# Kernel optimization log

Measured on AMD Instinct MI355X. Metric: run time of the kernel, lower is better.

The kernel has to match this reference:

```python
import jax, jax.numpy as jnp
import numpy as np

EPS = 1e-5

def _bn_relu(x, gamma, beta):
    # BatchNorm2d in training mode: biased batch stats over (B, H, W)
    mu = jnp.mean(x, axis=(0, 2, 3), keepdims=True)
    var = jnp.mean((x - mu) ** 2, axis=(0, 2, 3), keepdims=True)
    xh = (x - mu) * jax.lax.rsqrt(var + EPS)
    return jax.nn.relu(xh * gamma[None, :, None, None] + beta[None, :, None, None])

def setup_inputs() -> dict:
    key = jax.random.key(0)
    ks = jax.random.split(key, 16)
    B, N, D = 4, 256, 256            # in_channels = 2*D = 512
    feats = jax.random.normal(ks[0], (B, 1 + 2 * N, D), dtype=jnp.float32)
    def lin(k, o, c):
        return jax.random.normal(k, (o, c), dtype=jnp.float32) * (1.0 / np.sqrt(c))
    return {
        "feats": feats,
        "W1": lin(ks[1], 256, 512), "b1": jnp.zeros((256,), jnp.float32),
        "g1": jnp.ones((256,), jnp.float32), "be1": jnp.zeros((256,), jnp.float32),
        "W2": lin(ks[2], 128, 256), "b2": jnp.zeros((128,), jnp.float32),
        "g2": jnp.ones((128,), jnp.float32), "be2": jnp.zeros((128,), jnp.float32),
        "W3": lin(ks[3], 64, 128), "b3": jnp.zeros((64,), jnp.float32),
        "g3": jnp.ones((64,), jnp.float32), "be3": jnp.zeros((64,), jnp.float32),
        "W4": lin(ks[4], 1, 64), "b4": jnp.zeros((1,), jnp.float32),
    }

def reference(feats, W1, b1, g1, be1, W2, b2, g2, be2, W3, b3, g3, be3, W4, b4):
    B, T, Dfull = feats.shape
    f = feats[:, 1:]                                  # [B, 2N, D]
    N = f.shape[1] // 2
    D = f.shape[2]
    f = f.reshape(B, N, 2, D).mean(axis=2)            # [B, N, D]
    fc = jnp.transpose(f, (0, 2, 1))                  # [B, D, N]
    # conv1(cat(x, t)) fused: first D input channels see f_i, last D see f_j
    a = jnp.einsum('oc,bcn->bon', W1[:, :D], fc)      # [B, 256, N]
    bpart = jnp.einsum('oc,bcn->bon', W1[:, D:], fc)  # [B, 256, N]
    h = a[:, :, :, None] + bpart[:, :, None, :] + b1[None, :, None, None]  # [B,256,N,N]
    h = _bn_relu(h, g1, be1)
    h = jnp.einsum('oc,bcij->boij', W2, h) + b2[None, :, None, None]
    h = _bn_relu(h, g2, be2)
    h = jnp.einsum('oc,bcij->boij', W3, h) + b3[None, :, None, None]
    h = _bn_relu(h, g3, be3)
    h = jnp.einsum('oc,bcij->boij', W4, h) + b4[None, :, None, None]
    return h[:, 0]                                    # [B, N, N]
```

## Files before the change

### kernel.cpp

```cpp
#include <hip/hip_runtime.h>
#include <hip/hip_bf16.h>

#define EPS 1e-5f

typedef __attribute__((ext_vector_type(8))) short bf16x8;
typedef __attribute__((ext_vector_type(4))) float f32x4;

static constexpr size_t OFF_FT    = 0;
static constexpr size_t OFF_W1T   = 1048576;
static constexpr size_t OFF_W2B   = 1572864;
static constexpr size_t OFF_W3B   = 1638400;
static constexpr size_t OFF_S1    = 1654784;
static constexpr size_t OFF_T1    = 1655808;
static constexpr size_t OFF_S2    = 1658368;
static constexpr size_t OFF_T2    = 1658880;
static constexpr size_t OFF_S3    = 1659392;
static constexpr size_t OFF_T3    = 1659648;
static constexpr size_t OFF_ST2   = 1660928;
static constexpr size_t OFF_ST3   = 1669120;
static constexpr size_t OFF_ABT   = 1703936;
static constexpr size_t OFF_H2T   = 4194304;
static constexpr size_t OFF_P1    = OFF_H2T;
static constexpr size_t OFF_H3T   = 71303168;

static __device__ inline float bfu2f(unsigned int u16) {
    return __uint_as_float(u16 << 16);
}
static __device__ inline unsigned short f2bfu(float f) {
    unsigned int u = __float_as_uint(f);
    unsigned int r = u + 0x7fffu + ((u >> 16) & 1u);
    return (unsigned short)(r >> 16);
}
static __device__ inline unsigned int pkbf(float lo, float hi) {
    __hip_bfloat162 p = __float22bfloat162_rn(make_float2(lo, hi));
    return *reinterpret_cast<unsigned int*>(&p);
}

static __device__ __forceinline__ uint2 bnpk4(float4 fv, const float* aa, const float* ss, int c) {
    float4 a4 = *(const float4*)(aa + c);
    float4 s4 = *(const float4*)(ss + c);
    float r0 = fmaxf(fmaf(fv.x, s4.x, a4.x), 0.f);
    float r1 = fmaxf(fmaf(fv.y, s4.y, a4.y), 0.f);
    float r2 = fmaxf(fmaf(fv.z, s4.z, a4.z), 0.f);
    float r3 = fmaxf(fmaf(fv.w, s4.w, a4.w), 0.f);
    return make_uint2(pkbf(r0, r1), pkbf(r2, r3));
}
static __device__ __forceinline__ uint2 bn2pk4(uint2 v, const float* ss, const float* tt, int c) {
    float4 s4 = *(const float4*)(ss + c);
    float4 t4 = *(const float4*)(tt + c);
    float r0 = fmaxf(fmaf(bfu2f(v.x & 0xffffu), s4.x, t4.x), 0.f);
    float r1 = fmaxf(fmaf(bfu2f(v.x >> 16),     s4.y, t4.y), 0.f);
    float r2 = fmaxf(fmaf(bfu2f(v.y & 0xffffu), s4.z, t4.z), 0.f);
    float r3 = fmaxf(fmaf(bfu2f(v.y >> 16),     s4.w, t4.w), 0.f);
    return make_uint2(pkbf(r0, r1), pkbf(r2, r3));
}

__global__ __launch_bounds__(256) void k0_pairmean_T(const float* __restrict__ feats,
                                                     float* __restrict__ fT) {
    __shared__ float s[32][65];
    int bx = blockIdx.x;
    int b = bx >> 5, nt = (bx >> 2) & 7, ct = bx & 3;
    int n0 = nt * 32, c0 = ct * 64;
    int tid = threadIdx.x;
    const float* fb = feats + (size_t)b * 513 * 256;
    #pragma unroll
    for (int k = 0; k < 8; ++k) {
        int idx = tid + k * 256;
        int n = idx >> 6, c = idx & 63;
        const float* r = fb + (size_t)(1 + 2 * (n0 + n)) * 256 + c0 + c;
        s[n][c] = 0.5f * (r[0] + r[256]);
    }
    __syncthreads();
    #pragma unroll
    for (int k = 0; k < 8; ++k) {
        int idx = tid + k * 256;
        int c = idx >> 5, n = idx & 31;
        fT[((size_t)(b * 256) + c0 + c) * 256 + n0 + n] = s[n][c];
    }
}

__global__ void kt_prep(const float* __restrict__ W1, const float* __restrict__ W2,
                        const float* __restrict__ W3, float* __restrict__ W1T,
                        unsigned short* __restrict__ W2b, unsigned short* __restrict__ W3b) {
    int idx = blockIdx.x * 256 + threadIdx.x;
    if (idx < 131072) {
        int c = idx >> 9, o = idx & 511;
        W1T[idx] = (o < 256) ? W1[(size_t)o * 512 + c] : W1[(size_t)(o - 256) * 512 + 256 + c];
    } else if (idx < 163840) {
        int j = idx - 131072;
        W2b[j] = f2bfu(W2[j]);
    } else if (idx < 172032) {
        int j = idx - 163840;
        W3b[j] = f2bfu(W3[j]);
    }
}

__global__ __launch_bounds__(256) void k1_gemm(const float* __restrict__ W1T,
                                               const float* __restrict__ fT,
                                               float* __restrict__ abT,
                                               float2* __restrict__ part) {
    __shared__ float sW[64][36];
    __shared__ float sF[64][68];
    int tid = threadIdx.x;
    int bx = blockIdx.x;
    int b = bx >> 2, n0 = (bx & 3) * 64;
    int o0 = blockIdx.y * 32;
    int og = tid >> 4, jq = tid & 15;
    float acc[2][4] = {};
    for (int c0 = 0; c0 < 256; c0 += 64) {
        #pragma unroll
        for (int k = 0; k < 8; ++k) {
            int idx = tid + k * 256;
            int c = idx >> 5, o = idx & 31;
            sW[c][o] = W1T[(size_t)(c0 + c) * 512 + o0 + o];
        }
        #pragma unroll
        for (int k = 0; k < 16; ++k) {
            int idx = tid + k * 256;
            int c = idx >> 6, n = idx & 63;
            sF[c][n] = fT[((size_t)(b * 256) + c0 + c) * 256 + n0 + n];
        }
        __syncthreads();
        #pragma unroll 8
        for (int c = 0; c < 64; ++c) {
            float4 rv = *(const float4*)&sF[c][jq * 4];
            float2 wv = *(const float2*)&sW[c][og * 2];
            float rr[4] = {rv.x, rv.y, rv.z, rv.w};
            #pragma unroll
            for (int w = 0; w < 4; ++w) {
                acc[0][w] = fmaf(wv.x, rr[w], acc[0][w]);
                acc[1][w] = fmaf(wv.y, rr[w], acc[1][w]);
            }
        }
        __syncthreads();
    }
    #pragma unroll
    for (int w = 0; w < 4; ++w) {
        int n = n0 + jq * 4 + w;
        *(float2*)&abT[((size_t)(b * 256) + n) * 512 + o0 + og * 2] =
            make_float2(acc[0][w], acc[1][w]);
    }
    #pragma unroll
    for (int m = 0; m < 2; ++m) {
        float s = 0.f, q = 0.f;
        #pragma unroll
        for (int w = 0; w < 4; ++w) { float v = acc[m][w]; s += v; q += v * v; }
        #pragma unroll
        for (int off = 8; off; off >>= 1) { s += __shfl_down(s, off); q += __shfl_down(q, off); }
        if (jq == 0) part[(size_t)bx * 512 + o0 + og * 2 + m] = make_float2(s, q);
    }
}

__global__ void k1b_stats(const float2* __restrict__ part, const float* __restrict__ g1,
                          const float* __restrict__ be1, float* __restrict__ s1,
                          float* __restrict__ t1) {
    __shared__ float Sl[4][512], Ql[4][512];
    int o = threadIdx.x;
    for (int b = 0; b < 4; ++b) {
        float s = 0.f, q = 0.f;
        #pragma unroll
        for (int nt = 0; nt < 4; ++nt) {
            float2 p = part[(size_t)(b * 4 + nt) * 512 + o];
            s += p.x; q += p.y;
        }
        Sl[b][o] = s; Ql[b][o] = q;
    }
    __syncthreads();
    if (o < 256) {
        float msum = 0.f, e2sum = 0.f;
        #pragma unroll
        for (int b = 0; b < 4; ++b) {
            float ma = Sl[b][o] * (1.f / 256.f), mb = Sl[b][o + 256] * (1.f / 256.f);
            msum += ma + mb;
            e2sum += Ql[b][o] * (1.f / 256.f) + Ql[b][o + 256] * (1.f / 256.f) + 2.f * ma * mb;
        }
        float m = msum * 0.25f, e2 = e2sum * 0.25f;
        float var = e2 - m * m;
        float s = g1[o] * rsqrtf(var + EPS);
        s1[o] = s;
        t1[o] = be1[o] - m * s;
    }
}

__global__ __launch_bounds__(256) void k2_mfma(const float* __restrict__ abT,
                                               const unsigned short* __restrict__ W2b,
                                               const float* __restrict__ s1,
                                               const float* __restrict__ t1,
                                               unsigned short* __restrict__ h2T,
                                               float* __restrict__ gS2,
                                               float* __restrict__ gQ2) {
    __shared__ __align__(16) char smem[23552];
    float* aaS = (float*)smem;
    float* ssS = (float*)(smem + 1024);
    float* sS  = (float*)(smem + 2048);
    float* sQ  = (float*)(smem + 2560);
    unsigned short* sB0 = (unsigned short*)(smem + 3072);
    unsigned short* sB1 = (unsigned short*)(smem + 13312);
    unsigned short* sT  = (unsigned short*)(smem + 3072);

    int tid = threadIdx.x;
    int j0 = blockIdx.x * 128, i = blockIdx.y, b = blockIdx.z;

    {
        float av = abT[((size_t)(b * 256 + i)) * 512 + tid];
        float s = s1[tid];
        aaS[tid] = fmaf(av, s, t1[tid]);
        ssS[tid] = s;
    }
    if (tid < 128) { sS[tid] = 0.f; sQ[tid] = 0.f; }
    __syncthreads();

    int lane = tid & 63, wv = tid >> 6;
    int wr = wv >> 1, wc = wv & 1;
    int lo = lane & 15, khi = lane >> 4;
    int jr = tid >> 1, half = tid & 1;

    const float* bpRow = abT + ((size_t)(b * 256 + j0 + jr)) * 512 + 256 + half * 16;
    const unsigned short* wBase = W2b + (wr * 64 + lo) * 256 + khi * 8;

    f32x4 acc[4][4] = {};
    bf16x8 af0, af1, af2, af3;

    {
        int c = half * 16;
        float4 f0 = *(const float4*)(bpRow + 0);
        float4 f1 = *(const float4*)(bpRow + 4);
        float4 f2 = *(const float4*)(bpRow + 8);
        float4 f3 = *(const float4*)(bpRow + 12);
        uint2 p0 = bnpk4(f0, aaS, ssS, c);
        uint2 p1 = bnpk4(f1, aaS, ssS, c + 4);
        uint2 p2 = bnpk4(f2, aaS, ssS, c + 8);
        uint2 p3 = bnpk4(f3, aaS, ssS, c + 12);
        *(uint4*)(sB0 + jr * 40 + half * 16)     = make_uint4(p0.x, p0.y, p1.x, p1.y);
        *(uint4*)(sB0 + jr * 40 + half * 16 + 8) = make_uint4(p2.x, p2.y, p3.x, p3.y);
    }
    af0 = *(const bf16x8*)(wBase);
    af1 = *(const bf16x8*)(wBase + 4096);
    af2 = *(const bf16x8*)(wBase + 8192);
    af3 = *(const bf16x8*)(wBase + 12288);
    __syncthreads();

    unsigned short* curB = sB0;
    unsigned short* nxtB = sB1;
    #pragma unroll 2
    for (int k = 0; k < 8; ++k) {
        int c0 = k * 32;
        float4 f0, f1, f2, f3;
        bf16x8 an0, an1, an2, an3;
        if (k < 7) {
            f0 = *(const float4*)(bpRow + c0 + 32);
            f1 = *(const float4*)(bpRow + c0 + 36);
            f2 = *(const float4*)(bpRow + c0 + 40);
            f3 = *(const float4*)(bpRow + c0 + 44);
            an0 = *(const bf16x8*)(wBase + c0 + 32);
            an1 = *(const bf16x8*)(wBase + 4096 + c0 + 32);
            an2 = *(const bf16x8*)(wBase + 8192 + c0 + 32);
            an3 = *(const bf16x8*)(wBase + 12288 + c0 + 32);
        }
        bf16x8 bfr[4];
        #pragma unroll
        for (int fn = 0; fn < 4; ++fn)
            bfr[fn] = *(const bf16x8*)(curB + (wc * 64 + fn * 16 + lo) * 40 + khi * 8);
        #pragma unroll
        for (int fn = 0; fn < 4; ++fn) {
            acc[0][fn] = __builtin_amdgcn_mfma_f32_16x16x32_bf16(af0, bfr[fn], acc[0][fn], 0, 0, 0);
            acc[1][fn] = __builtin_amdgcn_mfma_f32_16x16x32_bf16(af1, bfr[fn], acc[1][fn], 0, 0, 0);
            acc[2][fn] = __builtin_amdgcn_mfma_f32_16x16x32_bf16(af2, bfr[fn], acc[2][fn], 0, 0, 0);
            acc[3][fn] = __builtin_amdgcn_mfma_f32_16x16x32_bf16(af3, bfr[fn], acc[3][fn], 0, 0, 0);
        }
        if (k < 7) {
            int cn = c0 + 32 + half * 16;
            uint2 p0 = bnpk4(f0, aaS, ssS, cn);
            uint2 p1 = bnpk4(f1, aaS, ssS, cn + 4);
            uint2 p2 = bnpk4(f2, aaS, ssS, cn + 8);
            uint2 p3 = bnpk4(f3, aaS, ssS, cn + 12);
            *(uint4*)(nxtB + jr * 40 + half * 16)     = make_uint4(p0.x, p0.y, p1.x, p1.y);
            *(uint4*)(nxtB + jr * 40 + half * 16 + 8) = make_uint4(p2.x, p2.y, p3.x, p3.y);
            af0 = an0; af1 = an1; af2 = an2; af3 = an3;
        }
        __syncthreads();
        unsigned short* t = curB; curB = nxtB; nxtB = t;
    }

    #pragma unroll
    for (int fm = 0; fm < 4; ++fm)
        #pragma unroll
        for (int r = 0; r < 4; ++r) {
            float s = 0.f, q = 0.f;
            #pragma unroll
            for (int fn = 0; fn < 4; ++fn) { float v = acc[fm][fn][r]; s += v; q += v * v; }
            #pragma unroll
            for (int off = 8; off; off >>= 1) { s += __shfl_down(s, off); q += __shfl_down(q, off); }
            if (lo == 0) {
                int o = wr * 64 + fm * 16 + khi * 4 + r;
                atomicAdd(&sS[o], s);
                atomicAdd(&sQ[o], q);
            }
        }

    #pragma unroll
    for (int rr = 0; rr < 2; ++rr) {
        __syncthreads();
        if (wr == rr) {
            #pragma unroll
            for (int fm = 0; fm < 4; ++fm)
                #pragma unroll
                for (int fn = 0; fn < 4; ++fn) {
                    int oq = fm * 16 + khi * 4;
                    int j  = wc * 64 + fn * 16 + lo;
                    *(uint2*)(sT + j * 72 + oq) =
                        make_uint2(pkbf(acc[fm][fn][0], acc[fm][fn][1]),
                                   pkbf(acc[fm][fn][2], acc[fm][fn][3]));
                }
        }
        __syncthreads();
        size_t g = (((size_t)(b * 256 + i)) * 256 + j0 + jr) * 128 + rr * 64 + half * 32;
        #pragma unroll
        for (int e = 0; e < 4; ++e) {
            uint4 v = *(const uint4*)(sT + jr * 72 + half * 32 + e * 8);
            *(uint4*)(h2T + g + e * 8) = v;
        }
    }
    if (tid < 128) {
        int slot = (i & 7) * 128;
        atomicAdd(&gS2[slot + tid], sS[tid]);
        atomicAdd(&gQ2[slot + tid], sQ[tid]);
    }
}

__global__ void kbnparam(const float* __restrict__ gS, const float* __restrict__ gQ,
                         const float* __restrict__ g, const float* __restrict__ be,
                         float* __restrict__ s, float* __restrict__ t, int C, float invc) {
    int o = threadIdx.x;
    if (o < C) {
        float su = 0.f, qu = 0.f;
        #pragma unroll
        for (int k = 0; k < 8; ++k) { su += gS[k * C + o]; qu += gQ[k * C + o]; }
        float mean = su * invc;
        float var = qu * invc - mean * mean;
        float sc = g[o] * rsqrtf(var + EPS);
        s[o] = sc;
        t[o] = be[o] - mean * sc;
    }
}

__global__ __launch_bounds__(256) void k3_mfma(const unsigned short* __restrict__ h2T,
                                               const unsigned short* __restrict__ W3b,
                                               const float* __restrict__ s2,
                                               const float* __restrict__ t2,
                                               unsigned short* __restrict__ h3T,
                                               float* __restrict__ gS3,
                                               float* __restrict__ gQ3) {
    __shared__ __align__(16) char smem[22016];
    float* s2S = (float*)smem;
    float* t2S = (float*)(smem + 512);
    float* sS  = (float*)(smem + 1024);
    float* sQ  = (float*)(smem + 1280);
    unsigned short* sB0 = (unsigned short*)(smem + 1536);
    unsigned short* sB1 = (unsigned short*)(smem + 11776);
    unsigned short* sT  = (unsigned short*)(smem + 1536);

    int tid = threadIdx.x;
    int j0 = blockIdx.x * 128, i = blockIdx.y, b = blockIdx.z;
    if (tid < 128) { s2S[tid] = s2[tid]; t2S[tid] = t2[tid]; }
    if (tid < 64) { sS[tid] = 0.f; sQ[tid] = 0.f; }
    __syncthreads();

    int lane = tid & 63, wv = tid >> 6;
    int lo = lane & 15, khi = lane >> 4;
    int jr = tid >> 1, half = tid & 1;

    const unsigned short* srcRow = h2T + (((size_t)(b * 256 + i)) * 256 + j0 + jr) * 128 + half * 16;
    const unsigned short* wBase = W3b + lo * 128 + khi * 8;

    f32x4 acc[4][2] = {};
    bf16x8 af0, af1, af2, af3;

    {
        int c = half * 16;
        uint4 v0 = *(const uint4*)(srcRow);
        uint4 v1 = *(const uint4*)(srcRow + 8);
        uint2 p0 = bn2pk4(make_uint2(v0.x, v0.y), s2S, t2S, c);
        uint2 p1 = bn2pk4(make_uint2(v0.z, v0.w), s2S, t2S, c + 4);
        uint2 p2 = bn2pk4(make_uint2(v1.x, v1.y), s2S, t2S, c + 8);
        uint2 p3 = bn2pk4(make_uint2(v1.z, v1.w), s2S, t2S, c + 12);
        *(uint4*)(sB0 + jr * 40 + half * 16)     = make_uint4(p0.x, p0.y, p1.x, p1.y);
        *(uint4*)(sB0 + jr * 40 + half * 16 + 8) = make_uint4(p2.x, p2.y, p3.x, p3.y);
    }
    af0 = *(const bf16x8*)(wBase);
    af1 = *(const bf16x8*)(wBase + 2048);
    af2 = *(const bf16x8*)(wBase + 4096);
    af3 = *(const bf16x8*)(wBase + 6144);
    __syncthreads();

    unsigned short* curB = sB0;
    unsigned short* nxtB = sB1;
    #pragma unroll 2
    for (int k = 0; k < 4; ++k) {
        int c0 = k * 32;
        uint4 v0, v1;
        bf16x8 an0, an1, an2, an3;
        if (k < 3) {
            v0 = *(const uint4*)(srcRow + c0 + 32);
            v1 = *(const uint4*)(srcRow + c0 + 40);
            an0 = *(const bf16x8*)(wBase + c0 + 32);
            an1 = *(const bf16x8*)(wBase + 2048 + c0 + 32);
            an2 = *(const bf16x8*)(wBase + 4096 + c0 + 32);
            an3 = *(const bf16x8*)(wBase + 6144 + c0 + 32);
        }
        bf16x8 bfr[2];
        #pragma unroll
        for (int fn = 0; fn < 2; ++fn)
            bfr[fn] = *(const bf16x8*)(curB + (wv * 32 + fn * 16 + lo) * 40 + khi * 8);
        #pragma unroll
        for (int fn = 0; fn < 2; ++fn) {
            acc[0][fn] = __builtin_amdgcn_mfma_f32_16x16x32_bf16(af0, bfr[fn], acc[0][fn], 0, 0, 0);
            acc[1][fn] = __builtin_amdgcn_mfma_f32_16x16x32_bf16(af1, bfr[fn], acc[1][fn], 0, 0, 0);
            acc[2][fn] = __builtin_amdgcn_mfma_f32_16x16x32_bf16(af2, bfr[fn], acc[2][fn], 0, 0, 0);
            acc[3][fn] = __builtin_amdgcn_mfma_f32_16x16x32_bf16(af3, bfr[fn], acc[3][fn], 0, 0, 0);
        }
        if (k < 3) {
            int cn = c0 + 32 + half * 16;
            uint2 p0 = bn2pk4(make_uint2(v0.x, v0.y), s2S, t2S, cn);
            uint2 p1 = bn2pk4(make_uint2(v0.z, v0.w), s2S, t2S, cn + 4);
            uint2 p2 = bn2pk4(make_uint2(v1.x, v1.y), s2S, t2S, cn + 8);
            uint2 p3 = bn2pk4(make_uint2(v1.z, v1.w), s2S, t2S, cn + 12);
            *(uint4*)(nxtB + jr * 40 + half * 16)     = make_uint4(p0.x, p0.y, p1.x, p1.y);
            *(uint4*)(nxtB + jr * 40 + half * 16 + 8) = make_uint4(p2.x, p2.y, p3.x, p3.y);
            af0 = an0; af1 = an1; af2 = an2; af3 = an3;
        }
        __syncthreads();
        unsigned short* t = curB; curB = nxtB; nxtB = t;
    }

    #pragma unroll
    for (int fm = 0; fm < 4; ++fm)
        #pragma unroll
        for (int r = 0; r < 4; ++r) {
            float s = 0.f, q = 0.f;
            #pragma unroll
            for (int fn = 0; fn < 2; ++fn) { float v = acc[fm][fn][r]; s += v; q += v * v; }
            #pragma unroll
            for (int off = 8; off; off >>= 1) { s += __shfl_down(s, off); q += __shfl_down(q, off); }
            if (lo == 0) {
                int o = fm * 16 + khi * 4 + r;
                atomicAdd(&sS[o], s);
                atomicAdd(&sQ[o], q);
            }
        }
    __syncthreads();

    #pragma unroll
    for (int fm = 0; fm < 4; ++fm)
        #pragma unroll
        for (int fn = 0; fn < 2; ++fn) {
            int oq = fm * 16 + khi * 4;
            int j  = wv * 32 + fn * 16 + lo;
            *(uint2*)(sT + j * 72 + oq) =
                make_uint2(pkbf(acc[fm][fn][0], acc[fm][fn][1]),
                           pkbf(acc[fm][fn][2], acc[fm][fn][3]));
        }
    __syncthreads();
    {
        size_t g = (((size_t)(b * 256 + i)) * 256 + j0 + jr) * 64 + half * 32;
        #pragma unroll
        for (int e = 0; e < 4; ++e) {
            uint4 v = *(const uint4*)(sT + jr * 72 + half * 32 + e * 8);
            *(uint4*)(h3T + g + e * 8) = v;
        }
    }
    if (tid < 64) {
        int slot = (i & 7) * 64;
        atomicAdd(&gS3[slot + tid], sS[tid]);
        atomicAdd(&gQ3[slot + tid], sQ[tid]);
    }
}

__global__ __launch_bounds__(256) void k4_final(const unsigned short* __restrict__ h3T,
                                                const float* __restrict__ W4,
                                                const float* __restrict__ s3,
                                                const float* __restrict__ t3,
                                                const float* __restrict__ b4,
                                                float* __restrict__ out) {
    __shared__ __align__(16) char smem[37632];
    float* wS = (float*)smem;
    float* sS = (float*)(smem + 256);
    float* tS = (float*)(smem + 512);
    unsigned short* sL = (unsigned short*)(smem + 768);
    int tid = threadIdx.x;
    int i = blockIdx.x, b = blockIdx.y;
    if (tid < 64) { wS[tid] = W4[tid]; sS[tid] = s3[tid]; tS[tid] = t3[tid]; }
    const unsigned short* src = h3T + ((size_t)(b * 256 + i)) * 256 * 64;
    #pragma unroll
    for (int e = 0; e < 8; ++e) {
        int f = tid + 256 * e;
        uint4 v = *(const uint4*)(src + f * 8);
        *(uint4*)(sL + (f >> 3) * 72 + (f & 7) * 8) = v;
    }
    __syncthreads();
    float acc = 0.f;
    #pragma unroll
    for (int e = 0; e < 8; ++e) {
        uint4 v = *(const uint4*)(sL + tid * 72 + e * 8);
        unsigned int w[4] = {v.x, v.y, v.z, v.w};
        #pragma unroll
        for (int k = 0; k < 4; ++k) {
            int c = e * 8 + 2 * k;
            float f0 = bfu2f(w[k] & 0xffffu);
            float f1 = bfu2f(w[k] >> 16);
            acc += wS[c] * fmaxf(fmaf(f0, sS[c], tS[c]), 0.f);
            acc += wS[c + 1] * fmaxf(fmaf(f1, sS[c + 1], tS[c + 1]), 0.f);
        }
    }
    out[((size_t)(b * 256 + i)) * 256 + tid] = acc + b4[0];
}

extern "C" void kernel_launch(void* const* d_in, const int* in_sizes, int n_in,
                              void* d_out, int out_size, void* d_ws, size_t ws_size,
                              hipStream_t stream) {
    const float* feats = (const float*)d_in[0];
    const float* W1  = (const float*)d_in[1];
    const float* g1  = (const float*)d_in[3];
    const float* be1 = (const float*)d_in[4];
    const float* W2  = (const float*)d_in[5];
    const float* g2  = (const float*)d_in[7];
    const float* be2 = (const float*)d_in[8];
    const float* W3  = (const float*)d_in[9];
    const float* g3  = (const float*)d_in[11];
    const float* be3 = (const float*)d_in[12];
    const float* W4  = (const float*)d_in[13];
    const float* b4  = (const float*)d_in[14];

    char* ws = (char*)d_ws;
    float* fT   = (float*)(ws + OFF_FT);
    float* W1T  = (float*)(ws + OFF_W1T);
    unsigned short* W2b = (unsigned short*)(ws + OFF_W2B);
    unsigned short* W3b = (unsigned short*)(ws + OFF_W3B);
    float* abT  = (float*)(ws + OFF_ABT);
    float* s1   = (float*)(ws + OFF_S1);
    float* t1   = (float*)(ws + OFF_T1);
    float* gS2  = (float*)(ws + OFF_ST2);
    float* gQ2  = (float*)(ws + OFF_ST2 + 4096);
    float* gS3  = (float*)(ws + OFF_ST3);
    float* gQ3  = (float*)(ws + OFF_ST3 + 2048);
    float* s2 = (float*)(ws + OFF_S2);
    float* t2 = (float*)(ws + OFF_T2);
    float* s3 = (float*)(ws + OFF_S3);
    float* t3 = (float*)(ws + OFF_T3);
    float2* part = (float2*)(ws + OFF_P1);
    unsigned short* h2T = (unsigned short*)(ws + OFF_H2T);
    unsigned short* h3T = (unsigned short*)(ws + OFF_H3T);
    float* out = (float*)d_out;

    hipMemsetAsync(ws + OFF_ST2, 0, 12288, stream);

    k0_pairmean_T<<<128, 256, 0, stream>>>(feats, fT);
    kt_prep<<<672, 256, 0, stream>>>(W1, W2, W3, W1T, W2b, W3b);
    k1_gemm<<<dim3(16, 16), 256, 0, stream>>>(W1T, fT, abT, part);
    k1b_stats<<<1, 512, 0, stream>>>(part, g1, be1, s1, t1);
    k2_mfma<<<dim3(2, 256, 4), 256, 0, stream>>>(abT, W2b, s1, t1, h2T, gS2, gQ2);
    kbnparam<<<1, 128, 0, stream>>>(gS2, gQ2, g2, be2, s2, t2, 128, 1.f / 262144.f);
    k3_mfma<<<dim3(2, 256, 4), 256, 0, stream>>>(h2T, W3b, s2, t2, h3T, gS3, gQ3);
    kbnparam<<<1, 64, 0, stream>>>(gS3, gQ3, g3, be3, s3, t3, 64, 1.f / 262144.f);
    k4_final<<<dim3(256, 4), 256, 0, stream>>>(h3T, W4, s3, t3, b4, out);
}
```

Before: 244.1 us.

## Load B operands directly from global into MFMA fragments, dropping LDS staging

In k2 and k3 each lane now reads its B fragment (abT for k2, h2T for k3) straight from global memory in MFMA layout. It applies the BN+ReLU and bf16 packing in registers and feeds the result to MFMA directly. This removes the double-buffered LDS tiles, the per-iteration __syncthreads and the software prefetch, and the k loop is fully unrolled. In exchange, the 2 waves sharing a column block now each fetch the same B data, the BN transform is recomputed redundantly, and the explicit prefetch is gone, so more latency may be exposed.

```diff
diff --git a/kernel.cpp b/kernel.cpp
--- a/kernel.cpp
+++ b/kernel.cpp
@@ -36,24 +36,7 @@
     return *reinterpret_cast<unsigned int*>(&p);
 }
 
-static __device__ __forceinline__ uint2 bnpk4(float4 fv, const float* aa, const float* ss, int c) {
-    float4 a4 = *(const float4*)(aa + c);
-    float4 s4 = *(const float4*)(ss + c);
-    float r0 = fmaxf(fmaf(fv.x, s4.x, a4.x), 0.f);
-    float r1 = fmaxf(fmaf(fv.y, s4.y, a4.y), 0.f);
-    float r2 = fmaxf(fmaf(fv.z, s4.z, a4.z), 0.f);
-    float r3 = fmaxf(fmaf(fv.w, s4.w, a4.w), 0.f);
-    return make_uint2(pkbf(r0, r1), pkbf(r2, r3));
-}
-static __device__ __forceinline__ uint2 bn2pk4(uint2 v, const float* ss, const float* tt, int c) {
-    float4 s4 = *(const float4*)(ss + c);
-    float4 t4 = *(const float4*)(tt + c);
-    float r0 = fmaxf(fmaf(bfu2f(v.x & 0xffffu), s4.x, t4.x), 0.f);
-    float r1 = fmaxf(fmaf(bfu2f(v.x >> 16),     s4.y, t4.y), 0.f);
-    float r2 = fmaxf(fmaf(bfu2f(v.y & 0xffffu), s4.z, t4.z), 0.f);
-    float r3 = fmaxf(fmaf(bfu2f(v.y >> 16),     s4.w, t4.w), 0.f);
-    return make_uint2(pkbf(r0, r1), pkbf(r2, r3));
-}
+union BFU { uint4 u; bf16x8 v; };
 
 __global__ __launch_bounds__(256) void k0_pairmean_T(const float* __restrict__ feats,
                                                      float* __restrict__ fT) {
@@ -189,14 +172,12 @@
                                                unsigned short* __restrict__ h2T,
                                                float* __restrict__ gS2,
                                                float* __restrict__ gQ2) {
-    __shared__ __align__(16) char smem[23552];
+    __shared__ __align__(16) char smem[21504];
     float* aaS = (float*)smem;
     float* ssS = (float*)(smem + 1024);
     float* sS  = (float*)(smem + 2048);
     float* sQ  = (float*)(smem + 2560);
-    unsigned short* sB0 = (unsigned short*)(smem + 3072);
-    unsigned short* sB1 = (unsigned short*)(smem + 13312);
-    unsigned short* sT  = (unsigned short*)(smem + 3072);
+    unsigned short* sT = (unsigned short*)(smem + 3072);
 
     int tid = threadIdx.x;
     int j0 = blockIdx.x * 128, i = blockIdx.y, b = blockIdx.z;
@@ -215,71 +196,43 @@
     int lo = lane & 15, khi = lane >> 4;
     int jr = tid >> 1, half = tid & 1;
 
-    const float* bpRow = abT + ((size_t)(b * 256 + j0 + jr)) * 512 + 256 + half * 16;
     const unsigned short* wBase = W2b + (wr * 64 + lo) * 256 + khi * 8;
+    const float* bBase = abT + ((size_t)(b * 256) + j0 + wc * 64 + lo) * 512 + 256 + khi * 8;
 
     f32x4 acc[4][4] = {};
-    bf16x8 af0, af1, af2, af3;
-
-    {
-        int c = half * 16;
-        float4 f0 = *(const float4*)(bpRow + 0);
-        float4 f1 = *(const float4*)(bpRow + 4);
-        float4 f2 = *(const float4*)(bpRow + 8);
-        float4 f3 = *(const float4*)(bpRow + 12);
-        uint2 p0 = bnpk4(f0, aaS, ssS, c);
-        uint2 p1 = bnpk4(f1, aaS, ssS, c + 4);
-        uint2 p2 = bnpk4(f2, aaS, ssS, c + 8);
-        uint2 p3 = bnpk4(f3, aaS, ssS, c + 12);
-        *(uint4*)(sB0 + jr * 40 + half * 16)     = make_uint4(p0.x, p0.y, p1.x, p1.y);
-        *(uint4*)(sB0 + jr * 40 + half * 16 + 8) = make_uint4(p2.x, p2.y, p3.x, p3.y);
-    }
-    af0 = *(const bf16x8*)(wBase);
-    af1 = *(const bf16x8*)(wBase + 4096);
-    af2 = *(const bf16x8*)(wBase + 8192);
-    af3 = *(const bf16x8*)(wBase + 12288);
-    __syncthreads();
-
-    unsigned short* curB = sB0;
-    unsigned short* nxtB = sB1;
-    #pragma unroll 2
+
+    #pragma unroll
     for (int k = 0; k < 8; ++k) {
         int c0 = k * 32;
-        float4 f0, f1, f2, f3;
-        bf16x8 an0, an1, an2, an3;
-        if (k < 7) {
-            f0 = *(const float4*)(bpRow + c0 + 32);
-            f1 = *(const float4*)(bpRow + c0 + 36);
-            f2 = *(const float4*)(bpRow + c0 + 40);
-            f3 = *(const float4*)(bpRow + c0 + 44);
-            an0 = *(const bf16x8*)(wBase + c0 + 32);
-            an1 = *(const bf16x8*)(wBase + 4096 + c0 + 32);
-            an2 = *(const bf16x8*)(wBase + 8192 + c0 + 32);
-            an3 = *(const bf16x8*)(wBase + 12288 + c0 + 32);
-        }
-        bf16x8 bfr[4];
-        #pragma unroll
-        for (int fn = 0; fn < 4; ++fn)
-            bfr[fn] = *(const bf16x8*)(curB + (wc * 64 + fn * 16 + lo) * 40 + khi * 8);
+        int c = c0 + khi * 8;
+        float4 a0 = *(const float4*)&aaS[c];
+        float4 a1 = *(const float4*)&aaS[c + 4];
+        float4 s0 = *(const float4*)&ssS[c];
+        float4 s1v = *(const float4*)&ssS[c + 4];
+        bf16x8 af[4];
+        #pragma unroll
+        for (int fm = 0; fm < 4; ++fm)
+            af[fm] = *(const bf16x8*)(wBase + fm * 16 * 256 + c0);
         #pragma unroll
         for (int fn = 0; fn < 4; ++fn) {
-            acc[0][fn] = __builtin_amdgcn_mfma_f32_16x16x32_bf16(af0, bfr[fn], acc[0][fn], 0, 0, 0);
-            acc[1][fn] = __builtin_amdgcn_mfma_f32_16x16x32_bf16(af1, bfr[fn], acc[1][fn], 0, 0, 0);
-            acc[2][fn] = __builtin_amdgcn_mfma_f32_16x16x32_bf16(af2, bfr[fn], acc[2][fn], 0, 0, 0);
-            acc[3][fn] = __builtin_amdgcn_mfma_f32_16x16x32_bf16(af3, bfr[fn], acc[3][fn], 0, 0, 0);
-        }
-        if (k < 7) {
-            int cn = c0 + 32 + half * 16;
-            uint2 p0 = bnpk4(f0, aaS, ssS, cn);
-            uint2 p1 = bnpk4(f1, aaS, ssS, cn + 4);
-            uint2 p2 = bnpk4(f2, aaS, ssS, cn + 8);
-            uint2 p3 = bnpk4(f3, aaS, ssS, cn + 12);
-            *(uint4*)(nxtB + jr * 40 + half * 16)     = make_uint4(p0.x, p0.y, p1.x, p1.y);
-            *(uint4*)(nxtB + jr * 40 + half * 16 + 8) = make_uint4(p2.x, p2.y, p3.x, p3.y);
-            af0 = an0; af1 = an1; af2 = an2; af3 = an3;
-        }
-        __syncthreads();
-        unsigned short* t = curB; curB = nxtB; nxtB = t;
+            float4 u0 = *(const float4*)(bBase + fn * 8192 + c0);
+            float4 u1 = *(const float4*)(bBase + fn * 8192 + c0 + 4);
+            float r0 = fmaxf(fmaf(u0.x, s0.x, a0.x), 0.f);
+            float r1 = fmaxf(fmaf(u0.y, s0.y, a0.y), 0.f);
+            float r2 = fmaxf(fmaf(u0.z, s0.z, a0.z), 0.f);
+            float r3 = fmaxf(fmaf(u0.w, s0.w, a0.w), 0.f);
+            float r4 = fmaxf(fmaf(u1.x, s1v.x, a1.x), 0.f);
+            float r5 = fmaxf(fmaf(u1.y, s1v.y, a1.y), 0.f);
+            float r6 = fmaxf(fmaf(u1.z, s1v.z, a1.z), 0.f);
+            float r7 = fmaxf(fmaf(u1.w, s1v.w, a1.w), 0.f);
+            BFU cv;
+            cv.u = make_uint4(pkbf(r0, r1), pkbf(r2, r3), pkbf(r4, r5), pkbf(r6, r7));
+            bf16x8 bfr = cv.v;
+            acc[0][fn] = __builtin_amdgcn_mfma_f32_16x16x32_bf16(af[0], bfr, acc[0][fn], 0, 0, 0);
+            acc[1][fn] = __builtin_amdgcn_mfma_f32_16x16x32_bf16(af[1], bfr, acc[1][fn], 0, 0, 0);
+            acc[2][fn] = __builtin_amdgcn_mfma_f32_16x16x32_bf16(af[2], bfr, acc[2][fn], 0, 0, 0);
+            acc[3][fn] = __builtin_amdgcn_mfma_f32_16x16x32_bf16(af[3], bfr, acc[3][fn], 0, 0, 0);
+        }
     }
 
     #pragma unroll
@@ -351,14 +304,12 @@
                                                unsigned short* __restrict__ h3T,
                                                float* __restrict__ gS3,
                                                float* __restrict__ gQ3) {
-    __shared__ __align__(16) char smem[22016];
+    __shared__ __align__(16) char smem[19968];
     float* s2S = (float*)smem;
     float* t2S = (float*)(smem + 512);
     float* sS  = (float*)(smem + 1024);
     float* sQ  = (float*)(smem + 1280);
-    unsigned short* sB0 = (unsigned short*)(smem + 1536);
-    unsigned short* sB1 = (unsigned short*)(smem + 11776);
-    unsigned short* sT  = (unsigned short*)(smem + 1536);
+    unsigned short* sT = (unsigned short*)(smem + 1536);
 
     int tid = threadIdx.x;
     int j0 = blockIdx.x * 128, i = blockIdx.y, b = blockIdx.z;
@@ -370,67 +321,43 @@
     int lo = lane & 15, khi = lane >> 4;
     int jr = tid >> 1, half = tid & 1;
 
-    const unsigned short* srcRow = h2T + (((size_t)(b * 256 + i)) * 256 + j0 + jr) * 128 + half * 16;
     const unsigned short* wBase = W3b + lo * 128 + khi * 8;
+    const unsigned short* srcB = h2T + (((size_t)(b * 256 + i)) * 256 + j0 + wv * 32 + lo) * 128 + khi * 8;
 
     f32x4 acc[4][2] = {};
-    bf16x8 af0, af1, af2, af3;
-
-    {
-        int c = half * 16;
-        uint4 v0 = *(const uint4*)(srcRow);
-        uint4 v1 = *(const uint4*)(srcRow + 8);
-        uint2 p0 = bn2pk4(make_uint2(v0.x, v0.y), s2S, t2S, c);
-        uint2 p1 = bn2pk4(make_uint2(v0.z, v0.w), s2S, t2S, c + 4);
-        uint2 p2 = bn2pk4(make_uint2(v1.x, v1.y), s2S, t2S, c + 8);
-        uint2 p3 = bn2pk4(make_uint2(v1.z, v1.w), s2S, t2S, c + 12);
-        *(uint4*)(sB0 + jr * 40 + half * 16)     = make_uint4(p0.x, p0.y, p1.x, p1.y);
-        *(uint4*)(sB0 + jr * 40 + half * 16 + 8) = make_uint4(p2.x, p2.y, p3.x, p3.y);
-    }
-    af0 = *(const bf16x8*)(wBase);
-    af1 = *(const bf16x8*)(wBase + 2048);
-    af2 = *(const bf16x8*)(wBase + 4096);
-    af3 = *(const bf16x8*)(wBase + 6144);
-    __syncthreads();
-
-    unsigned short* curB = sB0;
-    unsigned short* nxtB = sB1;
-    #pragma unroll 2
+
+    #pragma unroll
     for (int k = 0; k < 4; ++k) {
         int c0 = k * 32;
-        uint4 v0, v1;
-        bf16x8 an0, an1, an2, an3;
-        if (k < 3) {
-            v0 = *(const uint4*)(srcRow + c0 + 32);
-            v1 = *(const uint4*)(srcRow + c0 + 40);
-            an0 = *(const bf16x8*)(wBase + c0 + 32);
-            an1 = *(const bf16x8*)(wBase + 2048 + c0 + 32);
-            an2 = *(const bf16x8*)(wBase + 4096 + c0 + 32);
-            an3 = *(const bf16x8*)(wBase + 6144 + c0 + 32);
-        }
-        bf16x8 bfr[2];
-        #pragma unroll
-        for (int fn = 0; fn < 2; ++fn)
-            bfr[fn] = *(const bf16x8*)(curB + (wv * 32 + fn * 16 + lo) * 40 + khi * 8);
+        int c = c0 + khi * 8;
+        float4 s0 = *(const float4*)&s2S[c];
+        float4 s1v = *(const float4*)&s2S[c + 4];
+        float4 t0 = *(const float4*)&t2S[c];
+        float4 t1v = *(const float4*)&t2S[c + 4];
+        bf16x8 af[4];
+        #pragma unroll
+        for (int fm = 0; fm < 4; ++fm)
+            af[fm] = *(const bf16x8*)(wBase + fm * 16 * 128 + c0);
         #pragma unroll
         for (int fn = 0; fn < 2; ++fn) {
-            acc[0][fn] = __builtin_amdgcn_mfma_f32_16x16x32_bf16(af0, bfr[fn], acc[0][fn], 0, 0, 0);
-            acc[1][fn] = __builtin_amdgcn_mfma_f32_16x16x32_bf16(af1, bfr[fn], acc[1][fn], 0, 0, 0);
-            acc[2][fn] = __builtin_amdgcn_mfma_f32_16x16x32_bf16(af2, bfr[fn], acc[2][fn], 0, 0, 0);
-            acc[3][fn] = __builtin_amdgcn_mfma_f32_16x16x32_bf16(af3, bfr[fn], acc[3][fn], 0, 0, 0);
-        }
-        if (k < 3) {
-            int cn = c0 + 32 + half * 16;
-            uint2 p0 = bn2pk4(make_uint2(v0.x, v0.y), s2S, t2S, cn);
-            uint2 p1 = bn2pk4(make_uint2(v0.z, v0.w), s2S, t2S, cn + 4);
-            uint2 p2 = bn2pk4(make_uint2(v1.x, v1.y), s2S, t2S, cn + 8);
-            uint2 p3 = bn2pk4(make_uint2(v1.z, v1.w), s2S, t2S, cn + 12);
-            *(uint4*)(nxtB + jr * 40 + half * 16)     = make_uint4(p0.x, p0.y, p1.x, p1.y);
-            *(uint4*)(nxtB + jr * 40 + half * 16 + 8) = make_uint4(p2.x, p2.y, p3.x, p3.y);
-            af0 = an0; af1 = an1; af2 = an2; af3 = an3;
-        }
-        __syncthreads();
-        unsigned short* t = curB; curB = nxtB; nxtB = t;
+            BFU raw;
+            raw.v = *(const bf16x8*)(srcB + fn * 16 * 128 + c0);
+            float r0 = fmaxf(fmaf(bfu2f(raw.u.x & 0xffffu), s0.x, t0.x), 0.f);
+            float r1 = fmaxf(fmaf(bfu2f(raw.u.x >> 16),     s0.y, t0.y), 0.f);
+            float r2 = fmaxf(fmaf(bfu2f(raw.u.y & 0xffffu), s0.z, t0.z), 0.f);
+            float r3 = fmaxf(fmaf(bfu2f(raw.u.y >> 16),     s0.w, t0.w), 0.f);
+            float r4 = fmaxf(fmaf(bfu2f(raw.u.z & 0xffffu), s1v.x, t1v.x), 0.f);
+            float r5 = fmaxf(fmaf(bfu2f(raw.u.z >> 16),     s1v.y, t1v.y), 0.f);
+            float r6 = fmaxf(fmaf(bfu2f(raw.u.w & 0xffffu), s1v.z, t1v.z), 0.f);
+            float r7 = fmaxf(fmaf(bfu2f(raw.u.w >> 16),     s1v.w, t1v.w), 0.f);
+            BFU cv;
+            cv.u = make_uint4(pkbf(r0, r1), pkbf(r2, r3), pkbf(r4, r5), pkbf(r6, r7));
+            bf16x8 bfr = cv.v;
+            acc[0][fn] = __builtin_amdgcn_mfma_f32_16x16x32_bf16(af[0], bfr, acc[0][fn], 0, 0, 0);
+            acc[1][fn] = __builtin_amdgcn_mfma_f32_16x16x32_bf16(af[1], bfr, acc[1][fn], 0, 0, 0);
+            acc[2][fn] = __builtin_amdgcn_mfma_f32_16x16x32_bf16(af[2], bfr, acc[2][fn], 0, 0, 0);
+            acc[3][fn] = __builtin_amdgcn_mfma_f32_16x16x32_bf16(af[3], bfr, acc[3][fn], 0, 0, 0);
+        }
     }
 
     #pragma unroll
```

Measured after the change: 289.8 us. 1.19x slower.
